# Performance work log

Hardware: AMD Instinct MI355X
Metric: run time of the kernel (lower is better)

Reference implementation:

```python
import jax, jax.numpy as jnp
import numpy as np

LN2 = 0.69314718  # matches the 2ln2 constant in the original rbf()


def setup_inputs() -> dict:
    key = jax.random.key(0)
    domain_min = [-1.0, -1.0, -1.0]
    domain_max = [1.0, 1.0, 1.0]
    n = [12, 12, 12]
    codomain_dim = 128
    N = 200000

    axes = [jnp.linspace(domain_min[i], domain_max[i], n[i], dtype=jnp.float32)
            for i in range(len(n))]
    # torch.meshgrid default is 'ij' indexing
    grid = jnp.stack(jnp.meshgrid(*axes, indexing='ij'), axis=-1).reshape(-1, len(n))  # [G, 3]

    # rbf_width: mean nearest-neighbor distance on the grid (second-smallest per row)
    d = jnp.linalg.norm(grid[:, None, :] - grid[None, :, :], axis=-1)  # [G, G], G=1728 -> small
    width = jnp.sort(d, axis=1)[:, 1].mean()

    # interpolation matrix m and coeffs = solve(m, weight), as in __init__ (no_grad buffer)
    m = jnp.exp(-(d ** 2) / (width ** 2 / LN2))
    k1, k2 = jax.random.split(key)
    weight = jax.random.normal(k1, (grid.shape[0], codomain_dim), dtype=jnp.float32)
    coeffs = jnp.linalg.solve(m, weight)  # [G, C]

    x = jax.random.normal(k2, (N, len(n)), dtype=jnp.float32)  # [N, 3]
    return {"x": x, "grid": grid, "coeffs": coeffs, "width": width}


def reference(x, grid, coeffs, width):
    # Squared Euclidean distance via |a|^2 + |b|^2 - 2ab (avoids [N, G, 3] broadcast tensor).
    # rbf(d, w) = exp(-d^2 / (w^2 / ln2)); since it only uses d^2, skip the sqrt.
    x2 = jnp.sum(x * x, axis=-1, keepdims=True)          # [N, 1]
    g2 = jnp.sum(grid * grid, axis=-1)                   # [G]
    d2 = x2 + g2[None, :] - 2.0 * (x @ grid.T)           # [N, G]
    d2 = jnp.maximum(d2, 0.0)                            # numerical guard
    p = jnp.exp(-d2 * (LN2 / (width * width)))           # [N, G]
    return p @ coeffs                                    # [N, C]
```

## Files before the change

### kernel.cpp

```cpp
#include <hip/hip_runtime.h>
#include <stdint.h>


typedef _Float16 f16;
typedef _Float16 f16x8 __attribute__((ext_vector_type(8)));
typedef float f32x16 __attribute__((ext_vector_type(16)));

#define LN2F 0.69314718f
#define LOG2E 1.4426950408889634f

#define CD 128
#define KD 1728
#define NSTEP 108
#define BM 128

__global__ void prep_coeffs(const float* __restrict__ coeffs,
                            f16* __restrict__ ch, f16* __restrict__ cl) {
  int kp  = blockIdx.x * 2 + (threadIdx.x >> 7);
  int col = threadIdx.x & 127;
  int i   = kp / 144;
  int r   = kp - i * 144;
  int s   = r >> 4;
  int idx = r & 15;
  int hh  = idx >> 3;
  int b   = idx & 7;
  int j, k2;
  if (s < 6) { j = 2 * s + hh;                 k2 = b; }
  else       { j = 4 * (s - 6) + 2 * hh + (b >> 2); k2 = 8 + (b & 3); }
  float v = coeffs[(size_t)((i * 12 + j) * 12 + k2) * CD + col];
  f16 h = (f16)v;
  f16 l = (f16)(v - (float)h);
  size_t o = ((size_t)(kp >> 3) * CD + col) * 8 + (kp & 7);
  ch[o] = h;
  cl[o] = l;
}

union FU { uint32_t u[4]; f16x8 v; };

__global__ __launch_bounds__(256, 2) void rbf_gemm(
    const float* __restrict__ x,
    const float* __restrict__ width,
    const f16* __restrict__ ch, const f16* __restrict__ cl,
    float* __restrict__ out, int N) {
  __shared__ float E0[12 * BM];
  __shared__ float E1[12 * BM];

  const int t = threadIdx.x;
  const int lane = t & 63;
  const int wv   = t >> 6;
  const int rbase = blockIdx.x * BM;

  const float w = width[0];
  const float s2 = (LN2F * LOG2E) / (w * w);

  if (t < BM) {
    int rr = rbase + t; if (rr >= N) rr = N - 1;
    float x0 = x[(size_t)rr * 3 + 0];
    float x1 = x[(size_t)rr * 3 + 1];
#pragma unroll
    for (int k = 0; k < 12; ++k) {
      float g = (float)k * (2.0f / 11.0f) - 1.0f;
      float d0 = x0 - g;
      float d1 = x1 - g;
      E0[k * BM + t] = __builtin_amdgcn_exp2f(-d0 * d0 * s2);
      E1[k * BM + t] = __builtin_amdgcn_exp2f(-d1 * d1 * s2);
    }
  }

  const int l31 = lane & 31;
  const int hh  = lane >> 5;
  const int wvr = wv >> 1;
  const int wvc = wv & 1;
  const int rl0 = wvr * 64 + l31;
  const int rl1 = rl0 + 32;

  float e2a[2][12];
#pragma unroll
  for (int mi = 0; mi < 2; ++mi) {
    int rr = rbase + (mi ? rl1 : rl0); if (rr >= N) rr = N - 1;
    float x2v = x[(size_t)rr * 3 + 2];
#pragma unroll
    for (int k = 0; k < 12; ++k) {
      float g = (float)k * (2.0f / 11.0f) - 1.0f;
      float d = x2v - g;
      e2a[mi][k] = __builtin_amdgcn_exp2f(-d * d * s2);
    }
  }

  const char* gh = (const char*)ch + (size_t)(hh * 128 + wvc * 64 + l31) * 16;
  const char* gl = (const char*)cl + (size_t)(hh * 128 + wvc * 64 + l31) * 16;

  f16x8 cbh0, cbh1, cbl0, cbl1;
  cbh0 = *(const f16x8*)(gh + 0);
  cbh1 = *(const f16x8*)(gh + 512);
  cbl0 = *(const f16x8*)(gl + 0);
  cbl1 = *(const f16x8*)(gl + 512);

  __syncthreads();

  f32x16 acc[2][2];
  {
    f32x16 z;
#pragma unroll
    for (int q = 0; q < 16; ++q) z[q] = 0.f;
#pragma unroll
    for (int mi = 0; mi < 2; ++mi)
#pragma unroll
      for (int nn = 0; nn < 2; ++nn) acc[mi][nn] = z;
  }

#pragma unroll 1
  for (int i = 0; i < 12; ++i) {
    float e0m[2];
    e0m[0] = E0[i * BM + rl0];
    e0m[1] = E0[i * BM + rl1];

#pragma unroll
    for (int s = 0; s < 9; ++s) {
      const char* ph = gh + (s + 1) * 4096;
      const char* pl = gl + (s + 1) * 4096;
      f16x8 nbh0 = *(const f16x8*)(ph);
      f16x8 nbh1 = *(const f16x8*)(ph + 512);
      f16x8 nbl0 = *(const f16x8*)(pl);
      f16x8 nbl1 = *(const f16x8*)(pl + 512);

      FU ah[2], al[2];
#pragma unroll
      for (int mi = 0; mi < 2; ++mi) {
        int rl = mi ? rl1 : rl0;
        if (s < 6) {
          float ej0 = e0m[mi] * E1[(2 * s + 0) * BM + rl];
          float ej1 = e0m[mi] * E1[(2 * s + 1) * BM + rl];
          float es  = hh ? ej1 : ej0;
#pragma unroll
          for (int q = 0; q < 4; ++q) {
            float ea = e2a[mi][2 * q];
            float eb = e2a[mi][2 * q + 1];
            uint32_t hq, lq;
            asm("v_fma_mixlo_f16 %0, %1, %2, 0"
                : "=v"(hq) : "v"(es), "v"(ea));
            asm("v_fma_mixhi_f16 %0, %1, %2, 0"
                : "+v"(hq) : "v"(es), "v"(eb));
            asm("v_fma_mixlo_f16 %0, %1, %2, -%3 op_sel:[0,0,0] op_sel_hi:[0,0,1]"
                : "=v"(lq) : "v"(es), "v"(ea), "v"(hq));
            asm("v_fma_mixhi_f16 %0, %1, %2, -%3 op_sel:[0,0,1] op_sel_hi:[0,0,1]"
                : "+v"(lq) : "v"(es), "v"(eb), "v"(hq));
            ah[mi].u[q] = hq;
            al[mi].u[q] = lq;
          }
        } else {
          int J0 = 4 * (s - 6);
          float e0v = e0m[mi];
          float ej0 = e0v * E1[(J0 + 0) * BM + rl];
          float ej1 = e0v * E1[(J0 + 1) * BM + rl];
          float ej2 = e0v * E1[(J0 + 2) * BM + rl];
          float ej3 = e0v * E1[(J0 + 3) * BM + rl];
          float c01 = hh ? ej2 : ej0;
          float c23 = hh ? ej3 : ej1;
#pragma unroll
          for (int q = 0; q < 4; ++q) {
            float es = (q < 2) ? c01 : c23;
            float ea = e2a[mi][8 + 2 * (q & 1)];
            float eb = e2a[mi][9 + 2 * (q & 1)];
            uint32_t hq, lq;
            asm("v_fma_mixlo_f16 %0, %1, %2, 0"
                : "=v"(hq) : "v"(es), "v"(ea));
            asm("v_fma_mixhi_f16 %0, %1, %2, 0"
                : "+v"(hq) : "v"(es), "v"(eb));
            asm("v_fma_mixlo_f16 %0, %1, %2, -%3 op_sel:[0,0,0] op_sel_hi:[0,0,1]"
                : "=v"(lq) : "v"(es), "v"(ea), "v"(hq));
            asm("v_fma_mixhi_f16 %0, %1, %2, -%3 op_sel:[0,0,1] op_sel_hi:[0,0,1]"
                : "+v"(lq) : "v"(es), "v"(eb), "v"(hq));
            ah[mi].u[q] = hq;
            al[mi].u[q] = lq;
          }
        }
      }

#pragma unroll
      for (int mi = 0; mi < 2; ++mi) {
        acc[mi][0] = __builtin_amdgcn_mfma_f32_32x32x16_f16(ah[mi].v, cbh0, acc[mi][0], 0, 0, 0);
        acc[mi][1] = __builtin_amdgcn_mfma_f32_32x32x16_f16(ah[mi].v, cbh1, acc[mi][1], 0, 0, 0);
      }
#pragma unroll
      for (int mi = 0; mi < 2; ++mi) {
        acc[mi][0] = __builtin_amdgcn_mfma_f32_32x32x16_f16(al[mi].v, cbh0, acc[mi][0], 0, 0, 0);
        acc[mi][1] = __builtin_amdgcn_mfma_f32_32x32x16_f16(al[mi].v, cbh1, acc[mi][1], 0, 0, 0);
      }
#pragma unroll
      for (int mi = 0; mi < 2; ++mi) {
        acc[mi][0] = __builtin_amdgcn_mfma_f32_32x32x16_f16(ah[mi].v, cbl0, acc[mi][0], 0, 0, 0);
        acc[mi][1] = __builtin_amdgcn_mfma_f32_32x32x16_f16(ah[mi].v, cbl1, acc[mi][1], 0, 0, 0);
      }

      cbh0 = nbh0; cbh1 = nbh1; cbl0 = nbl0; cbl1 = nbl1;
    }
    gh += 9 * 4096;
    gl += 9 * 4096;
  }

#pragma unroll
  for (int mi = 0; mi < 2; ++mi)
#pragma unroll
    for (int nn = 0; nn < 2; ++nn)
#pragma unroll
      for (int q = 0; q < 16; ++q) {
        int row = rbase + wvr * 64 + mi * 32 + (q & 3) + 8 * (q >> 2) + 4 * hh;
        int col = wvc * 64 + nn * 32 + l31;
        if (row < N) out[(size_t)row * CD + col] = acc[mi][nn][q];
      }
}

__global__ void rbf_fallback(const float* __restrict__ x, const float* __restrict__ grid,
                             const float* __restrict__ coeffs, const float* __restrict__ width,
                             float* __restrict__ out, int N) {
  int row = blockIdx.x;
  int col = threadIdx.x;
  if (row >= N) return;
  float x0 = x[(size_t)row * 3 + 0];
  float x1 = x[(size_t)row * 3 + 1];
  float x2 = x[(size_t)row * 3 + 2];
  float w = width[0];
  float s2 = (LN2F * LOG2E) / (w * w);
  float acc = 0.f;
  for (int g = 0; g < 1728; ++g) {
    float d0 = x0 - grid[g * 3 + 0];
    float d1 = x1 - grid[g * 3 + 1];
    float d2 = x2 - grid[g * 3 + 2];
    float p = exp2f(-(d0 * d0 + d1 * d1 + d2 * d2) * s2);
    acc += p * coeffs[(size_t)g * CD + col];
  }
  out[(size_t)row * CD + col] = acc;
}

extern "C" void kernel_launch(void* const* d_in, const int* in_sizes, int n_in,
                              void* d_out, int out_size, void* d_ws, size_t ws_size,
                              hipStream_t stream) {
  const float* x      = (const float*)d_in[0];
  const float* grid   = (const float*)d_in[1];
  const float* coeffs = (const float*)d_in[2];
  const float* width  = (const float*)d_in[3];
  float* out = (float*)d_out;
  int N = in_sizes[0] / 3;

  size_t need = (size_t)2 * CD * KD * sizeof(f16) + 16384;
  if (ws_size >= need) {
    f16* ch = (f16*)d_ws;
    f16* cl = ch + (size_t)CD * KD;
    hipLaunchKernelGGL(prep_coeffs, dim3(KD / 2), dim3(256), 0, stream,
                       coeffs, ch, cl);
    int nb = (N + BM - 1) / BM;
    hipLaunchKernelGGL(rbf_gemm, dim3(nb), dim3(256), 0, stream,
                       x, width, ch, cl, out, N);
  } else {
    hipLaunchKernelGGL(rbf_fallback, dim3(N), dim3(CD), 0, stream,
                       x, grid, coeffs, width, out, N);
  }
}
```

Before: 250.3 us.

## Have each wave compute all 128 output columns, halving A-fragment construction

The block shrinks from four waves to two, and each wave now covers 64 rows by all 128 columns with eight accumulator tiles instead of four. Previously the two column-split waves for the same rows each rebuilt identical split-f16 RBF A fragments with fma_mix. The change removes that duplicated VALU work and reuses each A fragment across twice as many MFMAs. In exchange, accumulator and B-fragment register usage per wave roughly doubles, which may reduce occupancy or latency hiding.

```diff
diff --git a/kernel.cpp b/kernel.cpp
--- a/kernel.cpp
+++ b/kernel.cpp
@@ -11,7 +11,6 @@
 
 #define CD 128
 #define KD 1728
-#define NSTEP 108
 #define BM 128
 
 __global__ void prep_coeffs(const float* __restrict__ coeffs,
@@ -37,7 +36,7 @@
 
 union FU { uint32_t u[4]; f16x8 v; };
 
-__global__ __launch_bounds__(256, 2) void rbf_gemm(
+__global__ __launch_bounds__(128, 2) void rbf_gemm(
     const float* __restrict__ x,
     const float* __restrict__ width,
     const f16* __restrict__ ch, const f16* __restrict__ cl,
@@ -69,8 +68,7 @@
 
   const int l31 = lane & 31;
   const int hh  = lane >> 5;
-  const int wvr = wv >> 1;
-  const int wvc = wv & 1;
+  const int wvr = wv;
   const int rl0 = wvr * 64 + l31;
   const int rl1 = rl0 + 32;
 
@@ -87,18 +85,19 @@
     }
   }
 
-  const char* gh = (const char*)ch + (size_t)(hh * 128 + wvc * 64 + l31) * 16;
-  const char* gl = (const char*)cl + (size_t)(hh * 128 + wvc * 64 + l31) * 16;
-
-  f16x8 cbh0, cbh1, cbl0, cbl1;
-  cbh0 = *(const f16x8*)(gh + 0);
-  cbh1 = *(const f16x8*)(gh + 512);
-  cbl0 = *(const f16x8*)(gl + 0);
-  cbl1 = *(const f16x8*)(gl + 512);
+  const char* gh = (const char*)ch + (size_t)(hh * 128 + l31) * 16;
+  const char* gl = (const char*)cl + (size_t)(hh * 128 + l31) * 16;
+
+  f16x8 cbh[4], cbl[4];
+#pragma unroll
+  for (int nn = 0; nn < 4; ++nn) {
+    cbh[nn] = *(const f16x8*)(gh + nn * 512);
+    cbl[nn] = *(const f16x8*)(gl + nn * 512);
+  }
 
   __syncthreads();
 
-  f32x16 acc[2][2];
+  f32x16 acc[2][4];
   {
     f32x16 z;
 #pragma unroll
@@ -106,7 +105,7 @@
 #pragma unroll
     for (int mi = 0; mi < 2; ++mi)
 #pragma unroll
-      for (int nn = 0; nn < 2; ++nn) acc[mi][nn] = z;
+      for (int nn = 0; nn < 4; ++nn) acc[mi][nn] = z;
   }
 
 #pragma unroll 1
@@ -119,10 +118,12 @@
     for (int s = 0; s < 9; ++s) {
       const char* ph = gh + (s + 1) * 4096;
       const char* pl = gl + (s + 1) * 4096;
-      f16x8 nbh0 = *(const f16x8*)(ph);
-      f16x8 nbh1 = *(const f16x8*)(ph + 512);
-      f16x8 nbl0 = *(const f16x8*)(pl);
-      f16x8 nbl1 = *(const f16x8*)(pl + 512);
+      f16x8 nbh[4], nbl[4];
+#pragma unroll
+      for (int nn = 0; nn < 4; ++nn) {
+        nbh[nn] = *(const f16x8*)(ph + nn * 512);
+        nbl[nn] = *(const f16x8*)(pl + nn * 512);
+      }
 
       FU ah[2], al[2];
 #pragma unroll
@@ -178,22 +179,23 @@
       }
 
 #pragma unroll
-      for (int mi = 0; mi < 2; ++mi) {
-        acc[mi][0] = __builtin_amdgcn_mfma_f32_32x32x16_f16(ah[mi].v, cbh0, acc[mi][0], 0, 0, 0);
-        acc[mi][1] = __builtin_amdgcn_mfma_f32_32x32x16_f16(ah[mi].v, cbh1, acc[mi][1], 0, 0, 0);
-      }
-#pragma unroll
-      for (int mi = 0; mi < 2; ++mi) {
-        acc[mi][0] = __builtin_amdgcn_mfma_f32_32x32x16_f16(al[mi].v, cbh0, acc[mi][0], 0, 0, 0);
-        acc[mi][1] = __builtin_amdgcn_mfma_f32_32x32x16_f16(al[mi].v, cbh1, acc[mi][1], 0, 0, 0);
-      }
-#pragma unroll
-      for (int mi = 0; mi < 2; ++mi) {
-        acc[mi][0] = __builtin_amdgcn_mfma_f32_32x32x16_f16(ah[mi].v, cbl0, acc[mi][0], 0, 0, 0);
-        acc[mi][1] = __builtin_amdgcn_mfma_f32_32x32x16_f16(ah[mi].v, cbl1, acc[mi][1], 0, 0, 0);
-      }
-
-      cbh0 = nbh0; cbh1 = nbh1; cbl0 = nbl0; cbl1 = nbl1;
+      for (int nn = 0; nn < 4; ++nn)
+#pragma unroll
+        for (int mi = 0; mi < 2; ++mi)
+          acc[mi][nn] = __builtin_amdgcn_mfma_f32_32x32x16_f16(ah[mi].v, cbh[nn], acc[mi][nn], 0, 0, 0);
+#pragma unroll
+      for (int nn = 0; nn < 4; ++nn)
+#pragma unroll
+        for (int mi = 0; mi < 2; ++mi)
+          acc[mi][nn] = __builtin_amdgcn_mfma_f32_32x32x16_f16(al[mi].v, cbh[nn], acc[mi][nn], 0, 0, 0);
+#pragma unroll
+      for (int nn = 0; nn < 4; ++nn)
+#pragma unroll
+        for (int mi = 0; mi < 2; ++mi)
+          acc[mi][nn] = __builtin_amdgcn_mfma_f32_32x32x16_f16(ah[mi].v, cbl[nn], acc[mi][nn], 0, 0, 0);
+
+#pragma unroll
+      for (int nn = 0; nn < 4; ++nn) { cbh[nn] = nbh[nn]; cbl[nn] = nbl[nn]; }
     }
     gh += 9 * 4096;
     gl += 9 * 4096;
@@ -202,11 +204,11 @@
 #pragma unroll
   for (int mi = 0; mi < 2; ++mi)
 #pragma unroll
-    for (int nn = 0; nn < 2; ++nn)
+    for (int nn = 0; nn < 4; ++nn)
 #pragma unroll
       for (int q = 0; q < 16; ++q) {
         int row = rbase + wvr * 64 + mi * 32 + (q & 3) + 8 * (q >> 2) + 4 * hh;
-        int col = wvc * 64 + nn * 32 + l31;
+        int col = nn * 32 + l31;
         if (row < N) out[(size_t)row * CD + col] = acc[mi][nn][q];
       }
 }
@@ -250,7 +252,7 @@
     hipLaunchKernelGGL(prep_coeffs, dim3(KD / 2), dim3(256), 0, stream,
                        coeffs, ch, cl);
     int nb = (N + BM - 1) / BM;
-    hipLaunchKernelGGL(rbf_gemm, dim3(nb), dim3(256), 0, stream,
+    hipLaunchKernelGGL(rbf_gemm, dim3(nb), dim3(128), 0, stream,
                        x, width, ch, cl, out, N);
   } else {
     hipLaunchKernelGGL(rbf_fallback, dim3(N), dim3(CD), 0, stream,
```

Result: slower. 258.7 us (+3.4%).

## Halve row tile per block and drop shared-memory exp tables for register-computed factors

Applied to the files above, without the earlier changes.

Shrinks each block from 128 to 64 rows, so each wave handles one 32-row MFMA tile instead of two. The E0/E1 separable exponential tables move from shared memory into registers computed per thread, which removes LDS traffic and the block barrier. It also removes the occupancy hint from launch bounds. The cost is half the reuse of every coefficient load (twice the global/L2 traffic for coeffs per output row) and more blocks, in exchange for fewer registers and higher occupancy.

```diff
diff --git a/kernel.cpp b/kernel.cpp
--- a/kernel.cpp
+++ b/kernel.cpp
@@ -11,8 +11,6 @@
 
 #define CD 128
 #define KD 1728
-#define NSTEP 108
-#define BM 128
 
 __global__ void prep_coeffs(const float* __restrict__ coeffs,
                             f16* __restrict__ ch, f16* __restrict__ cl) {
@@ -37,83 +35,56 @@
 
 union FU { uint32_t u[4]; f16x8 v; };
 
-__global__ __launch_bounds__(256, 2) void rbf_gemm(
+__global__ __launch_bounds__(256) void rbf_gemm(
     const float* __restrict__ x,
     const float* __restrict__ width,
     const f16* __restrict__ ch, const f16* __restrict__ cl,
     float* __restrict__ out, int N) {
-  __shared__ float E0[12 * BM];
-  __shared__ float E1[12 * BM];
-
-  const int t = threadIdx.x;
+  const int t    = threadIdx.x;
   const int lane = t & 63;
   const int wv   = t >> 6;
-  const int rbase = blockIdx.x * BM;
-
-  const float w = width[0];
+  const int l31  = lane & 31;
+  const int hh   = lane >> 5;
+  const int wvr  = wv >> 1;
+  const int wvc  = wv & 1;
+  const int rbase = blockIdx.x * 64;
+
+  const float w  = width[0];
   const float s2 = (LN2F * LOG2E) / (w * w);
 
-  if (t < BM) {
-    int rr = rbase + t; if (rr >= N) rr = N - 1;
-    float x0 = x[(size_t)rr * 3 + 0];
-    float x1 = x[(size_t)rr * 3 + 1];
-#pragma unroll
-    for (int k = 0; k < 12; ++k) {
-      float g = (float)k * (2.0f / 11.0f) - 1.0f;
-      float d0 = x0 - g;
-      float d1 = x1 - g;
-      E0[k * BM + t] = __builtin_amdgcn_exp2f(-d0 * d0 * s2);
-      E1[k * BM + t] = __builtin_amdgcn_exp2f(-d1 * d1 * s2);
-    }
-  }
-
-  const int l31 = lane & 31;
-  const int hh  = lane >> 5;
-  const int wvr = wv >> 1;
-  const int wvc = wv & 1;
-  const int rl0 = wvr * 64 + l31;
-  const int rl1 = rl0 + 32;
-
-  float e2a[2][12];
-#pragma unroll
-  for (int mi = 0; mi < 2; ++mi) {
-    int rr = rbase + (mi ? rl1 : rl0); if (rr >= N) rr = N - 1;
-    float x2v = x[(size_t)rr * 3 + 2];
-#pragma unroll
-    for (int k = 0; k < 12; ++k) {
-      float g = (float)k * (2.0f / 11.0f) - 1.0f;
-      float d = x2v - g;
-      e2a[mi][k] = __builtin_amdgcn_exp2f(-d * d * s2);
-    }
+  int rr = rbase + wvr * 32 + l31;
+  if (rr >= N) rr = N - 1;
+  const float x0 = x[(size_t)rr * 3 + 0];
+  const float x1 = x[(size_t)rr * 3 + 1];
+  const float x2 = x[(size_t)rr * 3 + 2];
+
+  float e1a[12], e2a[12];
+#pragma unroll
+  for (int k = 0; k < 12; ++k) {
+    float g  = (float)k * (2.0f / 11.0f) - 1.0f;
+    float d1 = x1 - g;
+    float d2 = x2 - g;
+    e1a[k] = __builtin_amdgcn_exp2f(-d1 * d1 * s2);
+    e2a[k] = __builtin_amdgcn_exp2f(-d2 * d2 * s2);
   }
 
   const char* gh = (const char*)ch + (size_t)(hh * 128 + wvc * 64 + l31) * 16;
   const char* gl = (const char*)cl + (size_t)(hh * 128 + wvc * 64 + l31) * 16;
 
-  f16x8 cbh0, cbh1, cbl0, cbl1;
-  cbh0 = *(const f16x8*)(gh + 0);
-  cbh1 = *(const f16x8*)(gh + 512);
-  cbl0 = *(const f16x8*)(gl + 0);
-  cbl1 = *(const f16x8*)(gl + 512);
-
-  __syncthreads();
-
-  f32x16 acc[2][2];
-  {
-    f32x16 z;
-#pragma unroll
-    for (int q = 0; q < 16; ++q) z[q] = 0.f;
-#pragma unroll
-    for (int mi = 0; mi < 2; ++mi)
-#pragma unroll
-      for (int nn = 0; nn < 2; ++nn) acc[mi][nn] = z;
-  }
+  f16x8 cbh0 = *(const f16x8*)(gh);
+  f16x8 cbh1 = *(const f16x8*)(gh + 512);
+  f16x8 cbl0 = *(const f16x8*)(gl);
+  f16x8 cbl1 = *(const f16x8*)(gl + 512);
+
+  f32x16 acc0, acc1;
+#pragma unroll
+  for (int q = 0; q < 16; ++q) { acc0[q] = 0.f; acc1[q] = 0.f; }
 
 #pragma unroll 1
   for (int i = 0; i < 12; ++i) {
-    float e0m[2];
-    e0m[0] = E0[i * BM + rl0];
-    e0m[1] = E0[i * BM + rl1];
+    float gi  = (float)i * (2.0f / 11.0f) - 1.0f;
+    float d0  = x0 - gi;
+    float e0i = __builtin_amdgcn_exp2f(-d0 * d0 * s2);
 
 #pragma unroll
     for (int s = 0; s < 9; ++s) {
@@ -124,74 +95,54 @@
       f16x8 nbl0 = *(const f16x8*)(pl);
       f16x8 nbl1 = *(const f16x8*)(pl + 512);
 
-      FU ah[2], al[2];
-#pragma unroll
-      for (int mi = 0; mi < 2; ++mi) {
-        int rl = mi ? rl1 : rl0;
-        if (s < 6) {
-          float ej0 = e0m[mi] * E1[(2 * s + 0) * BM + rl];
-          float ej1 = e0m[mi] * E1[(2 * s + 1) * BM + rl];
-          float es  = hh ? ej1 : ej0;
-#pragma unroll
-          for (int q = 0; q < 4; ++q) {
-            float ea = e2a[mi][2 * q];
-            float eb = e2a[mi][2 * q + 1];
-            uint32_t hq, lq;
-            asm("v_fma_mixlo_f16 %0, %1, %2, 0"
-                : "=v"(hq) : "v"(es), "v"(ea));
-            asm("v_fma_mixhi_f16 %0, %1, %2, 0"
-                : "+v"(hq) : "v"(es), "v"(eb));
-            asm("v_fma_mixlo_f16 %0, %1, %2, -%3 op_sel:[0,0,0] op_sel_hi:[0,0,1]"
-                : "=v"(lq) : "v"(es), "v"(ea), "v"(hq));
-            asm("v_fma_mixhi_f16 %0, %1, %2, -%3 op_sel:[0,0,1] op_sel_hi:[0,0,1]"
-                : "+v"(lq) : "v"(es), "v"(eb), "v"(hq));
-            ah[mi].u[q] = hq;
-            al[mi].u[q] = lq;
-          }
-        } else {
-          int J0 = 4 * (s - 6);
-          float e0v = e0m[mi];
-          float ej0 = e0v * E1[(J0 + 0) * BM + rl];
-          float ej1 = e0v * E1[(J0 + 1) * BM + rl];
-          float ej2 = e0v * E1[(J0 + 2) * BM + rl];
-          float ej3 = e0v * E1[(J0 + 3) * BM + rl];
-          float c01 = hh ? ej2 : ej0;
-          float c23 = hh ? ej3 : ej1;
-#pragma unroll
-          for (int q = 0; q < 4; ++q) {
-            float es = (q < 2) ? c01 : c23;
-            float ea = e2a[mi][8 + 2 * (q & 1)];
-            float eb = e2a[mi][9 + 2 * (q & 1)];
-            uint32_t hq, lq;
-            asm("v_fma_mixlo_f16 %0, %1, %2, 0"
-                : "=v"(hq) : "v"(es), "v"(ea));
-            asm("v_fma_mixhi_f16 %0, %1, %2, 0"
-                : "+v"(hq) : "v"(es), "v"(eb));
-            asm("v_fma_mixlo_f16 %0, %1, %2, -%3 op_sel:[0,0,0] op_sel_hi:[0,0,1]"
-                : "=v"(lq) : "v"(es), "v"(ea), "v"(hq));
-            asm("v_fma_mixhi_f16 %0, %1, %2, -%3 op_sel:[0,0,1] op_sel_hi:[0,0,1]"
-                : "+v"(lq) : "v"(es), "v"(eb), "v"(hq));
-            ah[mi].u[q] = hq;
-            al[mi].u[q] = lq;
-          }
+      FU ah, al;
+      if (s < 6) {
+        float es = e0i * (hh ? e1a[2 * s + 1] : e1a[2 * s]);
+#pragma unroll
+        for (int q = 0; q < 4; ++q) {
+          float ea = e2a[2 * q];
+          float eb = e2a[2 * q + 1];
+          uint32_t hq, lq;
+          asm("v_fma_mixlo_f16 %0, %1, %2, 0"
+              : "=v"(hq) : "v"(es), "v"(ea));
+          asm("v_fma_mixhi_f16 %0, %1, %2, 0"
+              : "+v"(hq) : "v"(es), "v"(eb));
+          asm("v_fma_mixlo_f16 %0, %1, %2, -%3 op_sel:[0,0,0] op_sel_hi:[0,0,1]"
+              : "=v"(lq) : "v"(es), "v"(ea), "v"(hq));
+          asm("v_fma_mixhi_f16 %0, %1, %2, -%3 op_sel:[0,0,1] op_sel_hi:[0,0,1]"
+              : "+v"(lq) : "v"(es), "v"(eb), "v"(hq));
+          ah.u[q] = hq;
+          al.u[q] = lq;
+        }
+      } else {
+        int J0 = 4 * (s - 6);
+        float c01 = e0i * (hh ? e1a[J0 + 2] : e1a[J0 + 0]);
+        float c23 = e0i * (hh ? e1a[J0 + 3] : e1a[J0 + 1]);
+#pragma unroll
+        for (int q = 0; q < 4; ++q) {
+          float es = (q < 2) ? c01 : c23;
+          float ea = e2a[8 + 2 * (q & 1)];
+          float eb = e2a[9 + 2 * (q & 1)];
+          uint32_t hq, lq;
+          asm("v_fma_mixlo_f16 %0, %1, %2, 0"
+              : "=v"(hq) : "v"(es), "v"(ea));
+          asm("v_fma_mixhi_f16 %0, %1, %2, 0"
+              : "+v"(hq) : "v"(es), "v"(eb));
+          asm("v_fma_mixlo_f16 %0, %1, %2, -%3 op_sel:[0,0,0] op_sel_hi:[0,0,1]"
+              : "=v"(lq) : "v"(es), "v"(ea), "v"(hq));
+          asm("v_fma_mixhi_f16 %0, %1, %2, -%3 op_sel:[0,0,1] op_sel_hi:[0,0,1]"
+              : "+v"(lq) : "v"(es), "v"(eb), "v"(hq));
+          ah.u[q] = hq;
+          al.u[q] = lq;
         }
       }
 
-#pragma unroll
-      for (int mi = 0; mi < 2; ++mi) {
-        acc[mi][0] = __builtin_amdgcn_mfma_f32_32x32x16_f16(ah[mi].v, cbh0, acc[mi][0], 0, 0, 0);
-        acc[mi][1] = __builtin_amdgcn_mfma_f32_32x32x16_f16(ah[mi].v, cbh1, acc[mi][1], 0, 0, 0);
-      }
-#pragma unroll
-      for (int mi = 0; mi < 2; ++mi) {
-        acc[mi][0] = __builtin_amdgcn_mfma_f32_32x32x16_f16(al[mi].v, cbh0, acc[mi][0], 0, 0, 0);
-        acc[mi][1] = __builtin_amdgcn_mfma_f32_32x32x16_f16(al[mi].v, cbh1, acc[mi][1], 0, 0, 0);
-      }
-#pragma unroll
-      for (int mi = 0; mi < 2; ++mi) {
-        acc[mi][0] = __builtin_amdgcn_mfma_f32_32x32x16_f16(ah[mi].v, cbl0, acc[mi][0], 0, 0, 0);
-        acc[mi][1] = __builtin_amdgcn_mfma_f32_32x32x16_f16(ah[mi].v, cbl1, acc[mi][1], 0, 0, 0);
-      }
+      acc0 = __builtin_amdgcn_mfma_f32_32x32x16_f16(ah.v, cbh0, acc0, 0, 0, 0);
+      acc1 = __builtin_amdgcn_mfma_f32_32x32x16_f16(ah.v, cbh1, acc1, 0, 0, 0);
+      acc0 = __builtin_amdgcn_mfma_f32_32x32x16_f16(al.v, cbh0, acc0, 0, 0, 0);
+      acc1 = __builtin_amdgcn_mfma_f32_32x32x16_f16(al.v, cbh1, acc1, 0, 0, 0);
+      acc0 = __builtin_amdgcn_mfma_f32_32x32x16_f16(ah.v, cbl0, acc0, 0, 0, 0);
+      acc1 = __builtin_amdgcn_mfma_f32_32x32x16_f16(ah.v, cbl1, acc1, 0, 0, 0);
 
       cbh0 = nbh0; cbh1 = nbh1; cbl0 = nbl0; cbl1 = nbl1;
     }
@@ -200,15 +151,14 @@
   }
 
 #pragma unroll
-  for (int mi = 0; mi < 2; ++mi)
-#pragma unroll
-    for (int nn = 0; nn < 2; ++nn)
-#pragma unroll
-      for (int q = 0; q < 16; ++q) {
-        int row = rbase + wvr * 64 + mi * 32 + (q & 3) + 8 * (q >> 2) + 4 * hh;
-        int col = wvc * 64 + nn * 32 + l31;
-        if (row < N) out[(size_t)row * CD + col] = acc[mi][nn][q];
-      }
+  for (int q = 0; q < 16; ++q) {
+    int row = rbase + wvr * 32 + (q & 3) + 8 * (q >> 2) + 4 * hh;
+    if (row < N) {
+      int col = wvc * 64 + l31;
+      out[(size_t)row * CD + col]      = acc0[q];
+      out[(size_t)row * CD + col + 32] = acc1[q];
+    }
+  }
 }
 
 __global__ void rbf_fallback(const float* __restrict__ x, const float* __restrict__ grid,
@@ -249,7 +199,7 @@
     f16* cl = ch + (size_t)CD * KD;
     hipLaunchKernelGGL(prep_coeffs, dim3(KD / 2), dim3(256), 0, stream,
                        coeffs, ch, cl);
-    int nb = (N + BM - 1) / BM;
+    int nb = (N + 63) / 64;
     hipLaunchKernelGGL(rbf_gemm, dim3(nb), dim3(256), 0, stream,
                        x, width, ch, cl, out, N);
   } else {
```

Result: slower. 283.2 us (+13.2%).
